# Kernel optimization log

Hardware: AMD Instinct MI355X
Metric: run time of the kernel (lower is better)

Reference implementation:

```python
import jax, jax.numpy as jnp
import numpy as np

B, C_IN, L, NCLASS = 256, 6, 512, 10

def setup_inputs() -> dict:
    key = jax.random.key(0)
    ks = jax.random.split(key, 16)
    g = lambda k, shp, s=0.05: jax.random.normal(k, shp, dtype=jnp.float32) * s
    return {
        "x": jax.random.normal(ks[0], (B, C_IN, L), dtype=jnp.float32),
        "conv1_w": g(ks[1], (32, C_IN, 3)),
        "conv1_b": g(ks[2], (32,)),
        "bn1_g": jnp.ones((32,), jnp.float32),
        "bn1_b": jnp.zeros((32,), jnp.float32),
        "bn1_m": g(ks[3], (32,)),
        "bn1_v": jnp.abs(g(ks[4], (32,))) + 1.0,
        "conv2_w": g(ks[5], (64, 32, 3)),
        "conv2_b": g(ks[6], (64,)),
        "bn2_g": jnp.ones((64,), jnp.float32),
        "bn2_b": jnp.zeros((64,), jnp.float32),
        "bn2_m": g(ks[7], (64,)),
        "bn2_v": jnp.abs(g(ks[8], (64,))) + 1.0,
        "wq": g(ks[9], (64, 64)),
        "bq": g(ks[10], (64,)),
        "wk": g(ks[11], (64, 64)),
        "bk": g(ks[12], (64,)),
        "wv": g(ks[13], (64, 64)),
        "bv": g(ks[14], (64,)),
        "fc_w": g(ks[15], (NCLASS, 64)),
        "fc_b": jnp.zeros((NCLASS,), jnp.float32),
    }

def _conv1d(x, w, b):
    # x: [B, C, L], w: [O, C, 3], padding=1 -> same length
    y = jax.lax.conv_general_dilated(
        x, w, window_strides=(1,), padding=[(1, 1)],
        dimension_numbers=("NCH", "OIH", "NCH"))
    return y + b[None, :, None]

def _bn(x, g, b, m, v, eps=1e-5):
    # eval-mode BatchNorm1d over channel dim of [B, C, L]
    inv = g * jax.lax.rsqrt(v + eps)
    return x * inv[None, :, None] + (b - m * inv)[None, :, None]

def reference(x, conv1_w, conv1_b, bn1_g, bn1_b, bn1_m, bn1_v,
              conv2_w, conv2_b, bn2_g, bn2_b, bn2_m, bn2_v,
              wq, bq, wk, bk, wv, bv, fc_w, fc_b):
    h = jax.nn.relu(_bn(_conv1d(x, conv1_w, conv1_b), bn1_g, bn1_b, bn1_m, bn1_v))
    h = jax.nn.relu(_bn(_conv1d(h, conv2_w, conv2_b), bn2_g, bn2_b, bn2_m, bn2_v))
    h = h.transpose(0, 2, 1)                      # [B, L, 64]
    q = h @ wq.T + bq
    k = h @ wk.T + bk
    v = h @ wv.T + bv
    scores = jnp.einsum("bqd,bkd->bqk", q, k) / jnp.sqrt(jnp.float32(64.0))
    attn = jax.nn.softmax(scores, axis=-1)
    out = jnp.einsum("bqk,bkd->bqd", attn, v)     # [B, L, 64]
    pooled = out.mean(axis=1)                     # [B, 64]
    return pooled @ fc_w.T + fc_b                 # [B, n_class]
```

## Files before the change

### kernel.cpp

```cpp
#include <hip/hip_runtime.h>
#include <hip/hip_bf16.h>


#define NB 256
#define LL 512
#define CIN 6
#define NCLASS 10
#define SLAB 8192
#define QSC 0.18033688f

typedef __bf16 bf16x8 __attribute__((ext_vector_type(8)));
typedef float f32x4 __attribute__((ext_vector_type(4)));
typedef unsigned short us4 __attribute__((ext_vector_type(4)));
typedef unsigned short us8 __attribute__((ext_vector_type(8)));
typedef unsigned int u32x4 __attribute__((ext_vector_type(4)));

static __device__ __forceinline__ unsigned short f2b(float f) {
    __bf16 h = (__bf16)f;
    return __builtin_bit_cast(unsigned short, h);
}

__global__ __launch_bounds__(256) void prep_weights(
    const float* __restrict__ w1, const float* __restrict__ cb1,
    const float* __restrict__ g1, const float* __restrict__ be1,
    const float* __restrict__ m1, const float* __restrict__ v1,
    const float* __restrict__ w2, const float* __restrict__ cb2,
    const float* __restrict__ g2, const float* __restrict__ be2,
    const float* __restrict__ m2, const float* __restrict__ v2,
    const float* __restrict__ wq, const float* __restrict__ wk,
    const float* __restrict__ wv,
    unsigned short* __restrict__ w1p, float* __restrict__ b1f,
    unsigned short* __restrict__ w2p, float* __restrict__ b2f,
    unsigned short* __restrict__ wqp, unsigned short* __restrict__ wkp,
    unsigned short* __restrict__ wvp)
{
    const int tt = blockIdx.x * 256 + threadIdx.x;
    for (int idx = tt; idx < 1024; idx += 2048) {
        int c = idx >> 5, k = idx & 31;
        int dl = k >> 3, ci = k & 7;
        float inv = g1[c] * rsqrtf(v1[c] + 1e-5f);
        float val = (dl < 3 && ci < 6) ? w1[c * 18 + ci * 3 + dl] * inv : 0.f;
        w1p[idx] = f2b(val);
    }
    if (tt < 32) {
        float inv = g1[tt] * rsqrtf(v1[tt] + 1e-5f);
        b1f[tt] = be1[tt] + (cb1[tt] - m1[tt]) * inv;
    }
    for (int idx = tt; idx < 2048; idx += 2048) {
        int c2 = idx >> 5, ci = idx & 31;
        float inv = g2[c2] * rsqrtf(v2[c2] + 1e-5f);
        const float* wp = w2 + c2 * 96 + ci * 3;
        w2p[c2 * 96 +      ci] = f2b(wp[0] * inv);
        w2p[c2 * 96 + 32 + ci] = f2b(wp[1] * inv);
        w2p[c2 * 96 + 64 + ci] = f2b(wp[2] * inv);
    }
    if (tt >= 64 && tt < 128) {
        int c2 = tt - 64;
        float inv = g2[c2] * rsqrtf(v2[c2] + 1e-5f);
        b2f[c2] = be2[c2] + (cb2[c2] - m2[c2]) * inv;
    }
    for (int idx = tt; idx < 4096; idx += 2048) {
        int d = idx >> 6, k = idx & 63;
        int kc = k >> 5, quad = (k >> 3) & 3, e = k & 7;
        int ch = kc * 32 + (e >> 2) * 16 + quad * 4 + (e & 3);
        wqp[idx] = f2b(wq[d * 64 + ch] * QSC);
        wkp[idx] = f2b(wk[d * 64 + ch]);
        wvp[idx] = f2b(wv[d * 64 + ch]);
    }
}

__global__ __launch_bounds__(512, 2) void fused_all(
    const float* __restrict__ x,
    const unsigned short* __restrict__ w1p, const float* __restrict__ b1f,
    const unsigned short* __restrict__ w2p, const float* __restrict__ b2f,
    const unsigned short* __restrict__ wqp, const unsigned short* __restrict__ wkp,
    const unsigned short* __restrict__ wvp,
    const float* __restrict__ bq, const float* __restrict__ bk,
    const float* __restrict__ bvp,
    const float* __restrict__ fcw, const float* __restrict__ fcb,
    float* __restrict__ outp)
{
    const int b = blockIdx.x;
    const int t = threadIdx.x;
    const int w = t >> 6, lane = t & 63, quad = lane >> 4, lc = lane & 15;

    __shared__ __align__(16) char smem[16 * SLAB + 8192];
    unsigned short* xstage = (unsigned short*)(smem + 16 * SLAB);
    float* redw   = (float*)(smem + 16 * SLAB) + w * 64;
    float* pooled = (float*)(smem + 16 * SLAB + 4096);

    unsigned short* slab[2] = { (unsigned short*)(smem + (2 * w) * SLAB),
                                (unsigned short*)(smem + (2 * w + 1) * SLAB) };

    {
        us8 pk;
        #pragma unroll
        for (int ci = 0; ci < 6; ci++)
            pk[ci] = f2b(x[((size_t)b * CIN + ci) * LL + t]);
        pk[6] = 0; pk[7] = 0;
        *(us8*)&xstage[t * 8] = pk;
    }
    __syncthreads();

    {
        bf16x8 bW1[2];
        #pragma unroll
        for (int nt = 0; nt < 2; nt++)
            bW1[nt] = *(const bf16x8*)(w1p + (nt * 16 + lc) * 32 + quad * 8);
        f32x4 b1q[2];
        #pragma unroll
        for (int nt = 0; nt < 2; nt++)
            b1q[nt] = *(const f32x4*)&b1f[nt * 16 + quad * 4];
        #pragma unroll
        for (int sg = 0; sg < 2; sg++) {
            const int g = 2 * w + sg;
            unsigned short* h1sl = slab[sg];
            #pragma unroll
            for (int mt = 0; mt < 3; mt++) {
                int j = mt * 16 + lc;
                int P = g * 32 - 1 + j;
                int src = P + quad - 1;
                bool okx = (src >= 0) && (src < LL);
                int srcc = src < 0 ? 0 : (src > 511 ? 511 : src);
                u32x4 xv = *(const u32x4*)&xstage[srcc * 8];
                if (!okx) { xv[0] = 0u; xv[1] = 0u; xv[2] = 0u; xv[3] = 0u; }
                bf16x8 aX = __builtin_bit_cast(bf16x8, xv);
                bool pv = (P >= 0) && (P < LL);
                #pragma unroll
                for (int nt = 0; nt < 2; nt++) {
                    f32x4 z = {0.f, 0.f, 0.f, 0.f};
                    f32x4 h = __builtin_amdgcn_mfma_f32_16x16x32_bf16(bW1[nt], aX, z, 0, 0, 0);
                    us4 pk;
                    #pragma unroll
                    for (int r = 0; r < 4; r++) {
                        float y = h[r] + b1q[nt][r];
                        y = (pv && y > 0.f) ? y : 0.f;
                        pk[r] = f2b(y);
                    }
                    if (j < 34)
                        *(us4*)&h1sl[j * 40 + nt * 16 + quad * 4] = pk;
                }
            }
        }
    }

    bf16x8 bX[2][2][3];
    #pragma unroll
    for (int sg = 0; sg < 2; sg++)
        #pragma unroll
        for (int rt = 0; rt < 2; rt++)
            #pragma unroll
            for (int kc = 0; kc < 3; kc++)
                bX[sg][rt][kc] = *(const bf16x8*)&slab[sg][(rt * 16 + lc + kc) * 40 + quad * 8];

    f32x4 acc2[2][4][2];
    #pragma unroll
    for (int nt = 0; nt < 4; nt++) {
        bf16x8 aW0 = *(const bf16x8*)(w2p + (nt * 16 + lc) * 96 + quad * 8);
        bf16x8 aW1 = *(const bf16x8*)(w2p + (nt * 16 + lc) * 96 + 32 + quad * 8);
        bf16x8 aW2 = *(const bf16x8*)(w2p + (nt * 16 + lc) * 96 + 64 + quad * 8);
        #pragma unroll
        for (int sg = 0; sg < 2; sg++)
            #pragma unroll
            for (int rt = 0; rt < 2; rt++) {
                f32x4 a = {0.f, 0.f, 0.f, 0.f};
                a = __builtin_amdgcn_mfma_f32_16x16x32_bf16(aW0, bX[sg][rt][0], a, 0, 0, 0);
                a = __builtin_amdgcn_mfma_f32_16x16x32_bf16(aW1, bX[sg][rt][1], a, 0, 0, 0);
                acc2[sg][nt][rt] = __builtin_amdgcn_mfma_f32_16x16x32_bf16(aW2, bX[sg][rt][2], a, 0, 0, 0);
            }
    }

    bf16x8 aH[2][2][2];
    #pragma unroll
    for (int nt2 = 0; nt2 < 4; nt2++) {
        f32x4 bb2 = *(const f32x4*)&b2f[nt2 * 16 + quad * 4];
        #pragma unroll
        for (int sg = 0; sg < 2; sg++)
            #pragma unroll
            for (int rt = 0; rt < 2; rt++)
                #pragma unroll
                for (int reg = 0; reg < 4; reg++) {
                    float y = acc2[sg][nt2][rt][reg] + bb2[reg];
                    aH[sg][rt][nt2 >> 1][(nt2 & 1) * 4 + reg] = (__bf16)(y > 0.f ? y : 0.f);
                }
    }

    f32x4 bbq[4], bbk[4];
    #pragma unroll
    for (int nt = 0; nt < 4; nt++) {
        bbq[nt] = *(const f32x4*)&bq[nt * 16 + quad * 4];
        bbk[nt] = *(const f32x4*)&bk[nt * 16 + quad * 4];
    }

    bf16x8 aQ4[4][2];
    #pragma unroll
    for (int nt = 0; nt < 4; nt++) {
        bf16x8 aW0 = *(const bf16x8*)(wqp + (nt * 16 + lc) * 64 + quad * 8);
        bf16x8 aW1 = *(const bf16x8*)(wqp + (nt * 16 + lc) * 64 + 32 + quad * 8);
        #pragma unroll
        for (int sg = 0; sg < 2; sg++)
            #pragma unroll
            for (int rt = 0; rt < 2; rt++) {
                f32x4 a = {0.f, 0.f, 0.f, 0.f};
                a = __builtin_amdgcn_mfma_f32_16x16x32_bf16(aW0, aH[sg][rt][0], a, 0, 0, 0);
                a = __builtin_amdgcn_mfma_f32_16x16x32_bf16(aW1, aH[sg][rt][1], a, 0, 0, 0);
                #pragma unroll
                for (int reg = 0; reg < 4; reg++)
                    aQ4[sg * 2 + rt][nt >> 1][(nt & 1) * 4 + reg] =
                        (__bf16)(a[reg] + bbq[nt][reg] * QSC);
            }
    }

    #pragma unroll
    for (int kc = 0; kc < 2; kc++) {
        f32x4 Ck[2][2][2];
        #pragma unroll
        for (int j = 0; j < 2; j++) {
            int nt = kc * 2 + j;
            bf16x8 aW0 = *(const bf16x8*)(wkp + (nt * 16 + lc) * 64 + quad * 8);
            bf16x8 aW1 = *(const bf16x8*)(wkp + (nt * 16 + lc) * 64 + 32 + quad * 8);
            #pragma unroll
            for (int sg = 0; sg < 2; sg++)
                #pragma unroll
                for (int rt = 0; rt < 2; rt++) {
                    f32x4 a = {0.f, 0.f, 0.f, 0.f};
                    a = __builtin_amdgcn_mfma_f32_16x16x32_bf16(aW0, aH[sg][rt][0], a, 0, 0, 0);
                    Ck[j][sg][rt] = __builtin_amdgcn_mfma_f32_16x16x32_bf16(aW1, aH[sg][rt][1], a, 0, 0, 0);
                }
        }
        #pragma unroll
        for (int sg = 0; sg < 2; sg++)
            #pragma unroll
            for (int rt = 0; rt < 2; rt++) {
                us8 pk;
                #pragma unroll
                for (int e = 0; e < 8; e++) {
                    int j = e >> 2, reg = e & 3, nt = kc * 2 + j;
                    pk[e] = f2b(Ck[j][sg][rt][reg] + bbk[nt][reg]);
                }
                *(us8*)&slab[sg][((rt * 2 + kc) << 9) + lane * 8] = pk;
            }
    }

    #pragma unroll
    for (int nt = 0; nt < 4; nt++) {
        bf16x8 bW0 = *(const bf16x8*)(wvp + (nt * 16 + lc) * 64 + quad * 8);
        bf16x8 bW1 = *(const bf16x8*)(wvp + (nt * 16 + lc) * 64 + 32 + quad * 8);
        const float bvv = bvp[nt * 16 + lc];
        #pragma unroll
        for (int sg = 0; sg < 2; sg++) {
            f32x4 a0, a1;
            {
                f32x4 z = {0.f, 0.f, 0.f, 0.f};
                z = __builtin_amdgcn_mfma_f32_16x16x32_bf16(aH[sg][0][0], bW0, z, 0, 0, 0);
                a0 = __builtin_amdgcn_mfma_f32_16x16x32_bf16(aH[sg][0][1], bW1, z, 0, 0, 0);
            }
            {
                f32x4 z = {0.f, 0.f, 0.f, 0.f};
                z = __builtin_amdgcn_mfma_f32_16x16x32_bf16(aH[sg][1][0], bW0, z, 0, 0, 0);
                a1 = __builtin_amdgcn_mfma_f32_16x16x32_bf16(aH[sg][1][1], bW1, z, 0, 0, 0);
            }
            us8 pk;
            #pragma unroll
            for (int reg = 0; reg < 4; reg++) {
                pk[reg]     = f2b(a0[reg] + bvv);
                pk[4 + reg] = f2b(a1[reg] + bvv);
            }
            *(us8*)&slab[sg][2048 + nt * 512 + lane * 8] = pk;
        }
    }

    __syncthreads();

    f32x4 outacc[4][4];
    #pragma unroll
    for (int rt = 0; rt < 4; rt++)
        #pragma unroll
        for (int dt = 0; dt < 4; dt++) outacc[rt][dt] = (f32x4){0.f, 0.f, 0.f, 0.f};
    f32x4 accDen[4];
    #pragma unroll
    for (int rt = 0; rt < 4; rt++) accDen[rt] = (f32x4){0.f, 0.f, 0.f, 0.f};
    bf16x8 bOne;
    #pragma unroll
    for (int e = 0; e < 8; e++) bOne[e] = (__bf16)1.0f;

    bf16x8 bK2[2][2];
    {
        const unsigned short* sK = (const unsigned short*)smem;
        #pragma unroll
        for (int nt = 0; nt < 2; nt++)
            #pragma unroll
            for (int kc = 0; kc < 2; kc++)
                bK2[nt][kc] = *(const bf16x8*)&sK[((nt * 2 + kc) << 9) + lane * 8];
    }
    f32x4 sv[2][4];
    #pragma unroll
    for (int nt = 0; nt < 2; nt++)
        #pragma unroll
        for (int rt = 0; rt < 4; rt++) {
            f32x4 z = {0.f, 0.f, 0.f, 0.f};
            z = __builtin_amdgcn_mfma_f32_16x16x32_bf16(bK2[nt][0], aQ4[rt][0], z, 0, 0, 0);
            sv[nt][rt] = __builtin_amdgcn_mfma_f32_16x16x32_bf16(bK2[nt][1], aQ4[rt][1], z, 0, 0, 0);
        }

    for (int cc = 0; cc < 16; cc++) {
        const unsigned short* sV = (const unsigned short*)(smem + cc * SLAB + 4096);
        bf16x8 bV[4];
        #pragma unroll
        for (int dt = 0; dt < 4; dt++)
            bV[dt] = *(const bf16x8*)&sV[dt * 512 + lane * 8];
        if (cc < 15) {
            const unsigned short* sKn = (const unsigned short*)(smem + (cc + 1) * SLAB);
            #pragma unroll
            for (int nt = 0; nt < 2; nt++)
                #pragma unroll
                for (int kc = 0; kc < 2; kc++)
                    bK2[nt][kc] = *(const bf16x8*)&sKn[((nt * 2 + kc) << 9) + lane * 8];
        }
        bf16x8 aP[4];
        #pragma unroll
        for (int rt = 0; rt < 4; rt++)
            #pragma unroll
            for (int nt = 0; nt < 2; nt++)
                #pragma unroll
                for (int reg = 0; reg < 4; reg++)
                    aP[rt][nt * 4 + reg] = (__bf16)__builtin_amdgcn_exp2f(sv[nt][rt][reg]);
        __builtin_amdgcn_s_setprio(1);
        #pragma unroll
        for (int rt = 0; rt < 4; rt++) {
            #pragma unroll
            for (int dt = 0; dt < 4; dt++)
                outacc[rt][dt] = __builtin_amdgcn_mfma_f32_16x16x32_bf16(aP[rt], bV[dt], outacc[rt][dt], 0, 0, 0);
            accDen[rt] = __builtin_amdgcn_mfma_f32_16x16x32_bf16(aP[rt], bOne, accDen[rt], 0, 0, 0);
        }
        if (cc < 15) {
            #pragma unroll
            for (int nt = 0; nt < 2; nt++)
                #pragma unroll
                for (int rt = 0; rt < 4; rt++) {
                    f32x4 z = {0.f, 0.f, 0.f, 0.f};
                    z = __builtin_amdgcn_mfma_f32_16x16x32_bf16(bK2[nt][0], aQ4[rt][0], z, 0, 0, 0);
                    sv[nt][rt] = __builtin_amdgcn_mfma_f32_16x16x32_bf16(bK2[nt][1], aQ4[rt][1], z, 0, 0, 0);
                }
        }
        __builtin_amdgcn_s_setprio(0);
    }

    float rden[4][4];
    #pragma unroll
    for (int rt = 0; rt < 4; rt++)
        #pragma unroll
        for (int reg = 0; reg < 4; reg++)
            rden[rt][reg] = 1.0f / accDen[rt][reg];
    #pragma unroll
    for (int dt = 0; dt < 4; dt++) {
        float ps = 0.f;
        #pragma unroll
        for (int rt = 0; rt < 4; rt++)
            #pragma unroll
            for (int reg = 0; reg < 4; reg++)
                ps += outacc[rt][dt][reg] * rden[rt][reg];
        ps += __shfl_xor(ps, 16);
        ps += __shfl_xor(ps, 32);
        if (quad == 0) redw[dt * 16 + lc] = ps;
    }
    __syncthreads();
    if (t < 64) {
        float s = 0.f;
        #pragma unroll
        for (int ww = 0; ww < 8; ww++)
            s += *(const float*)(smem + 16 * SLAB + ww * 256 + t * 4);
        pooled[t] = s * (1.0f / 512.0f);
    }
    __syncthreads();
    if (t < NCLASS) {
        float acc = fcb[t];
        #pragma unroll
        for (int d = 0; d < 64; d++) acc += pooled[d] * fcw[t * 64 + d];
        outp[b * NCLASS + t] = acc;
    }
}

extern "C" void kernel_launch(void* const* d_in, const int* in_sizes, int n_in,
                              void* d_out, int out_size, void* d_ws, size_t ws_size,
                              hipStream_t stream)
{
    const float* x   = (const float*)d_in[0];
    const float* w1  = (const float*)d_in[1];
    const float* cb1 = (const float*)d_in[2];
    const float* g1  = (const float*)d_in[3];
    const float* be1 = (const float*)d_in[4];
    const float* m1  = (const float*)d_in[5];
    const float* v1  = (const float*)d_in[6];
    const float* w2  = (const float*)d_in[7];
    const float* cb2 = (const float*)d_in[8];
    const float* g2  = (const float*)d_in[9];
    const float* be2 = (const float*)d_in[10];
    const float* m2  = (const float*)d_in[11];
    const float* v2  = (const float*)d_in[12];
    const float* wq  = (const float*)d_in[13];
    const float* bq  = (const float*)d_in[14];
    const float* wk  = (const float*)d_in[15];
    const float* bk  = (const float*)d_in[16];
    const float* wv  = (const float*)d_in[17];
    const float* bv  = (const float*)d_in[18];
    const float* fcw = (const float*)d_in[19];
    const float* fcb = (const float*)d_in[20];
    float* out = (float*)d_out;

    char* ws = (char*)d_ws;
    unsigned short* w1p = (unsigned short*)(ws);
    float*          b1f = (float*)(ws + 2048u);
    float*          b2f = (float*)(ws + 2176u);
    unsigned short* w2p = (unsigned short*)(ws + 2432u);
    unsigned short* wqp = (unsigned short*)(ws + 14720u);
    unsigned short* wkp = (unsigned short*)(ws + 22912u);
    unsigned short* wvp = (unsigned short*)(ws + 31104u);

    prep_weights<<<dim3(8), 256, 0, stream>>>(w1, cb1, g1, be1, m1, v1,
                                              w2, cb2, g2, be2, m2, v2,
                                              wq, wk, wv,
                                              w1p, b1f, w2p, b2f, wqp, wkp, wvp);
    fused_all<<<dim3(NB), 512, 0, stream>>>(x, w1p, b1f, w2p, b2f,
                                            wqp, wkp, wvp,
                                            bq, bk, bv, fcw, fcb, out);
}
```

Before: 119.9 us.

## Fold weight preparation into main kernel and drop separate prep launch

Removes the prep_weights kernel. Each block now computes the BatchNorm-folded conv weights and biases into shared memory, and gathers Q/K/V weights from fp32 global memory with in-register bf16 conversion. This aims to remove the second kernel launch and its serialization gap. In exchange every block repeats the weight preparation work, shared memory use grows, and the Q bias scaling order changes slightly.

```diff
diff --git a/kernel.cpp b/kernel.cpp
--- a/kernel.cpp
+++ b/kernel.cpp
@@ -20,63 +20,27 @@
     return __builtin_bit_cast(unsigned short, h);
 }
 
-__global__ __launch_bounds__(256) void prep_weights(
+static __device__ __forceinline__ bf16x8 gather_w(const float* __restrict__ wrow,
+                                                  int base, int quad) {
+    f32x4 a = *(const f32x4*)(wrow + base + quad * 4);
+    f32x4 b = *(const f32x4*)(wrow + base + 16 + quad * 4);
+    bf16x8 r;
+    #pragma unroll
+    for (int e = 0; e < 4; e++) { r[e] = (__bf16)a[e]; r[4 + e] = (__bf16)b[e]; }
+    return r;
+}
+
+__global__ __launch_bounds__(512, 2) void fused_all(
+    const float* __restrict__ x,
     const float* __restrict__ w1, const float* __restrict__ cb1,
     const float* __restrict__ g1, const float* __restrict__ be1,
     const float* __restrict__ m1, const float* __restrict__ v1,
     const float* __restrict__ w2, const float* __restrict__ cb2,
     const float* __restrict__ g2, const float* __restrict__ be2,
     const float* __restrict__ m2, const float* __restrict__ v2,
-    const float* __restrict__ wq, const float* __restrict__ wk,
-    const float* __restrict__ wv,
-    unsigned short* __restrict__ w1p, float* __restrict__ b1f,
-    unsigned short* __restrict__ w2p, float* __restrict__ b2f,
-    unsigned short* __restrict__ wqp, unsigned short* __restrict__ wkp,
-    unsigned short* __restrict__ wvp)
-{
-    const int tt = blockIdx.x * 256 + threadIdx.x;
-    for (int idx = tt; idx < 1024; idx += 2048) {
-        int c = idx >> 5, k = idx & 31;
-        int dl = k >> 3, ci = k & 7;
-        float inv = g1[c] * rsqrtf(v1[c] + 1e-5f);
-        float val = (dl < 3 && ci < 6) ? w1[c * 18 + ci * 3 + dl] * inv : 0.f;
-        w1p[idx] = f2b(val);
-    }
-    if (tt < 32) {
-        float inv = g1[tt] * rsqrtf(v1[tt] + 1e-5f);
-        b1f[tt] = be1[tt] + (cb1[tt] - m1[tt]) * inv;
-    }
-    for (int idx = tt; idx < 2048; idx += 2048) {
-        int c2 = idx >> 5, ci = idx & 31;
-        float inv = g2[c2] * rsqrtf(v2[c2] + 1e-5f);
-        const float* wp = w2 + c2 * 96 + ci * 3;
-        w2p[c2 * 96 +      ci] = f2b(wp[0] * inv);
-        w2p[c2 * 96 + 32 + ci] = f2b(wp[1] * inv);
-        w2p[c2 * 96 + 64 + ci] = f2b(wp[2] * inv);
-    }
-    if (tt >= 64 && tt < 128) {
-        int c2 = tt - 64;
-        float inv = g2[c2] * rsqrtf(v2[c2] + 1e-5f);
-        b2f[c2] = be2[c2] + (cb2[c2] - m2[c2]) * inv;
-    }
-    for (int idx = tt; idx < 4096; idx += 2048) {
-        int d = idx >> 6, k = idx & 63;
-        int kc = k >> 5, quad = (k >> 3) & 3, e = k & 7;
-        int ch = kc * 32 + (e >> 2) * 16 + quad * 4 + (e & 3);
-        wqp[idx] = f2b(wq[d * 64 + ch] * QSC);
-        wkp[idx] = f2b(wk[d * 64 + ch]);
-        wvp[idx] = f2b(wv[d * 64 + ch]);
-    }
-}
-
-__global__ __launch_bounds__(512, 2) void fused_all(
-    const float* __restrict__ x,
-    const unsigned short* __restrict__ w1p, const float* __restrict__ b1f,
-    const unsigned short* __restrict__ w2p, const float* __restrict__ b2f,
-    const unsigned short* __restrict__ wqp, const unsigned short* __restrict__ wkp,
-    const unsigned short* __restrict__ wvp,
-    const float* __restrict__ bq, const float* __restrict__ bk,
-    const float* __restrict__ bvp,
+    const float* __restrict__ wq, const float* __restrict__ bq,
+    const float* __restrict__ wk, const float* __restrict__ bk,
+    const float* __restrict__ wv, const float* __restrict__ bv,
     const float* __restrict__ fcw, const float* __restrict__ fcb,
     float* __restrict__ outp)
 {
@@ -84,10 +48,16 @@
     const int t = threadIdx.x;
     const int w = t >> 6, lane = t & 63, quad = lane >> 4, lc = lane & 15;
 
-    __shared__ __align__(16) char smem[16 * SLAB + 8192];
-    unsigned short* xstage = (unsigned short*)(smem + 16 * SLAB);
-    float* redw   = (float*)(smem + 16 * SLAB) + w * 64;
-    float* pooled = (float*)(smem + 16 * SLAB + 4096);
+    __shared__ __align__(16) char smem[154368];
+    unsigned short* xstage = (unsigned short*)(smem + 131072);
+    unsigned short* w2f = (unsigned short*)(smem + 139264);
+    unsigned short* w1f = (unsigned short*)(smem + 151552);
+    float* b1fl  = (float*)(smem + 153600);
+    float* b2fl  = (float*)(smem + 153728);
+    float* inv1l = (float*)(smem + 153984);
+    float* inv2l = (float*)(smem + 154112);
+    float* redw   = (float*)(smem + 131072) + w * 64;
+    float* pooled = (float*)(smem + 131072 + 4096);
 
     unsigned short* slab[2] = { (unsigned short*)(smem + (2 * w) * SLAB),
                                 (unsigned short*)(smem + (2 * w + 1) * SLAB) };
@@ -100,17 +70,43 @@
         pk[6] = 0; pk[7] = 0;
         *(us8*)&xstage[t * 8] = pk;
     }
+    if (t < 32) {
+        float iv = g1[t] * rsqrtf(v1[t] + 1e-5f);
+        inv1l[t] = iv;
+        b1fl[t] = be1[t] + (cb1[t] - m1[t]) * iv;
+    } else if (t < 96) {
+        int c2 = t - 32;
+        float iv = g2[c2] * rsqrtf(v2[c2] + 1e-5f);
+        inv2l[c2] = iv;
+        b2fl[c2] = be2[c2] + (cb2[c2] - m2[c2]) * iv;
+    }
+    __syncthreads();
+
+    for (int idx = t; idx < 6144; idx += 512) {
+        int e = idx & 7, lane2 = (idx >> 3) & 63, f = idx >> 9;
+        int nt = f & 3, kc = f >> 2;
+        int q2 = lane2 >> 4, lc2 = lane2 & 15;
+        int c2 = nt * 16 + lc2, ci = q2 * 8 + e;
+        w2f[idx] = f2b(w2[c2 * 96 + ci * 3 + kc] * inv2l[c2]);
+    }
+    for (int idx = t; idx < 1024; idx += 512) {
+        int e = idx & 7, lane2 = (idx >> 3) & 63, nt = idx >> 9;
+        int q2 = lane2 >> 4, lc2 = lane2 & 15;
+        int c = nt * 16 + lc2;
+        float val = (q2 < 3 && e < 6) ? w1[c * 18 + e * 3 + q2] * inv1l[c] : 0.f;
+        w1f[idx] = f2b(val);
+    }
     __syncthreads();
 
     {
         bf16x8 bW1[2];
         #pragma unroll
         for (int nt = 0; nt < 2; nt++)
-            bW1[nt] = *(const bf16x8*)(w1p + (nt * 16 + lc) * 32 + quad * 8);
+            bW1[nt] = *(const bf16x8*)&w1f[nt * 512 + lane * 8];
         f32x4 b1q[2];
         #pragma unroll
         for (int nt = 0; nt < 2; nt++)
-            b1q[nt] = *(const f32x4*)&b1f[nt * 16 + quad * 4];
+            b1q[nt] = *(const f32x4*)&b1fl[nt * 16 + quad * 4];
         #pragma unroll
         for (int sg = 0; sg < 2; sg++) {
             const int g = 2 * w + sg;
@@ -156,9 +152,9 @@
     f32x4 acc2[2][4][2];
     #pragma unroll
     for (int nt = 0; nt < 4; nt++) {
-        bf16x8 aW0 = *(const bf16x8*)(w2p + (nt * 16 + lc) * 96 + quad * 8);
-        bf16x8 aW1 = *(const bf16x8*)(w2p + (nt * 16 + lc) * 96 + 32 + quad * 8);
-        bf16x8 aW2 = *(const bf16x8*)(w2p + (nt * 16 + lc) * 96 + 64 + quad * 8);
+        bf16x8 aW0 = *(const bf16x8*)&w2f[(0 * 4 + nt) * 512 + lane * 8];
+        bf16x8 aW1 = *(const bf16x8*)&w2f[(1 * 4 + nt) * 512 + lane * 8];
+        bf16x8 aW2 = *(const bf16x8*)&w2f[(2 * 4 + nt) * 512 + lane * 8];
         #pragma unroll
         for (int sg = 0; sg < 2; sg++)
             #pragma unroll
@@ -173,7 +169,7 @@
     bf16x8 aH[2][2][2];
     #pragma unroll
     for (int nt2 = 0; nt2 < 4; nt2++) {
-        f32x4 bb2 = *(const f32x4*)&b2f[nt2 * 16 + quad * 4];
+        f32x4 bb2 = *(const f32x4*)&b2fl[nt2 * 16 + quad * 4];
         #pragma unroll
         for (int sg = 0; sg < 2; sg++)
             #pragma unroll
@@ -195,8 +191,9 @@
     bf16x8 aQ4[4][2];
     #pragma unroll
     for (int nt = 0; nt < 4; nt++) {
-        bf16x8 aW0 = *(const bf16x8*)(wqp + (nt * 16 + lc) * 64 + quad * 8);
-        bf16x8 aW1 = *(const bf16x8*)(wqp + (nt * 16 + lc) * 64 + 32 + quad * 8);
+        const float* wqr = wq + (nt * 16 + lc) * 64;
+        bf16x8 aW0 = gather_w(wqr, 0, quad);
+        bf16x8 aW1 = gather_w(wqr, 32, quad);
         #pragma unroll
         for (int sg = 0; sg < 2; sg++)
             #pragma unroll
@@ -207,7 +204,7 @@
                 #pragma unroll
                 for (int reg = 0; reg < 4; reg++)
                     aQ4[sg * 2 + rt][nt >> 1][(nt & 1) * 4 + reg] =
-                        (__bf16)(a[reg] + bbq[nt][reg] * QSC);
+                        (__bf16)((a[reg] + bbq[nt][reg]) * QSC);
             }
     }
 
@@ -217,8 +214,9 @@
         #pragma unroll
         for (int j = 0; j < 2; j++) {
             int nt = kc * 2 + j;
-            bf16x8 aW0 = *(const bf16x8*)(wkp + (nt * 16 + lc) * 64 + quad * 8);
-            bf16x8 aW1 = *(const bf16x8*)(wkp + (nt * 16 + lc) * 64 + 32 + quad * 8);
+            const float* wkr = wk + (nt * 16 + lc) * 64;
+            bf16x8 aW0 = gather_w(wkr, 0, quad);
+            bf16x8 aW1 = gather_w(wkr, 32, quad);
             #pragma unroll
             for (int sg = 0; sg < 2; sg++)
                 #pragma unroll
@@ -244,9 +242,10 @@
 
     #pragma unroll
     for (int nt = 0; nt < 4; nt++) {
-        bf16x8 bW0 = *(const bf16x8*)(wvp + (nt * 16 + lc) * 64 + quad * 8);
-        bf16x8 bW1 = *(const bf16x8*)(wvp + (nt * 16 + lc) * 64 + 32 + quad * 8);
-        const float bvv = bvp[nt * 16 + lc];
+        const float* wvr = wv + (nt * 16 + lc) * 64;
+        bf16x8 bW0 = gather_w(wvr, 0, quad);
+        bf16x8 bW1 = gather_w(wvr, 32, quad);
+        const float bvv = bv[nt * 16 + lc];
         #pragma unroll
         for (int sg = 0; sg < 2; sg++) {
             f32x4 a0, a1;
@@ -369,7 +368,7 @@
         float s = 0.f;
         #pragma unroll
         for (int ww = 0; ww < 8; ww++)
-            s += *(const float*)(smem + 16 * SLAB + ww * 256 + t * 4);
+            s += *(const float*)(smem + 131072 + ww * 256 + t * 4);
         pooled[t] = s * (1.0f / 512.0f);
     }
     __syncthreads();
@@ -407,21 +406,11 @@
     const float* fcw = (const float*)d_in[19];
     const float* fcb = (const float*)d_in[20];
     float* out = (float*)d_out;
-
-    char* ws = (char*)d_ws;
-    unsigned short* w1p = (unsigned short*)(ws);
-    float*          b1f = (float*)(ws + 2048u);
-    float*          b2f = (float*)(ws + 2176u);
-    unsigned short* w2p = (unsigned short*)(ws + 2432u);
-    unsigned short* wqp = (unsigned short*)(ws + 14720u);
-    unsigned short* wkp = (unsigned short*)(ws + 22912u);
-    unsigned short* wvp = (unsigned short*)(ws + 31104u);
-
-    prep_weights<<<dim3(8), 256, 0, stream>>>(w1, cb1, g1, be1, m1, v1,
-                                              w2, cb2, g2, be2, m2, v2,
-                                              wq, wk, wv,
-                                              w1p, b1f, w2p, b2f, wqp, wkp, wvp);
-    fused_all<<<dim3(NB), 512, 0, stream>>>(x, w1p, b1f, w2p, b2f,
-                                            wqp, wkp, wvp,
-                                            bq, bk, bv, fcw, fcb, out);
+    (void)d_ws; (void)ws_size;
+
+    fused_all<<<dim3(NB), 512, 0, stream>>>(x,
+                                            w1, cb1, g1, be1, m1, v1,
+                                            w2, cb2, g2, be2, m2, v2,
+                                            wq, bq, wk, bk, wv, bv,
+                                            fcw, fcb, out);
 }
```

Measured after the change: 124.4 us. 3.8% more time.
